# Performance work log

Measured on AMD Instinct MI355X. Metric: run time of the kernel, lower is better.

Reference implementation:

```python
import jax, jax.numpy as jnp
import numpy as np

B, IN_CS = 2, 32
H = W = D = 96

def conv1x1(w, v):
    # 1x1x1 Conv3d without bias: per-voxel matvec over channels
    return jnp.einsum('oc,bcxyz->boxyz', w, v)

def kron(a, b):
    # per-voxel outer product over channels; index order i*c2+j matches torch view
    bs, c1 = a.shape[:2]
    c2 = b.shape[1]
    out = jnp.einsum('bixyz,bjxyz->bijxyz', a, b)
    return out.reshape(bs, c1 * c2, *a.shape[2:])

def setup_inputs() -> dict:
    key = jax.random.key(0)
    ks = jax.random.split(key, 7)
    s = 0.1  # weight init scale
    return {
        'x': jax.random.normal(ks[0], (B, IN_CS, H, W, D), jnp.float32),
        'd_all': jax.random.normal(ks[1], (B, 6, H, W, D), jnp.float32),
        'W1': jax.random.normal(ks[2], (16, 2), jnp.float32) * s,
        'W2': jax.random.normal(ks[3], (3, 16), jnp.float32) * s,
        'G1': jax.random.normal(ks[4], (IN_CS, 27), jnp.float32) * s,
        'G2': jax.random.normal(ks[5], (2 * IN_CS, IN_CS), jnp.float32) * s,
        'G3': jax.random.normal(ks[6], (IN_CS, 2 * IN_CS), jnp.float32) * s,
    }

def reference(x, d_all, W1, W2, G1, G2, G3):
    def encode(v):
        return conv1x1(W2, jax.nn.relu(conv1x1(W1, v)))
    x_x = encode(d_all[:, 0:2])
    y_y = encode(d_all[:, 2:4])
    z_z = encode(d_all[:, 4:6])
    enced = kron(kron(x_x, y_y), z_z)  # [B, 27, H, W, D]
    h = jax.nn.relu(conv1x1(G1, enced))
    h = jax.nn.relu(conv1x1(G2, h))
    filters = conv1x1(G3, h)  # [B, IN_CS, H, W, D]
    return jnp.sum(x * filters, axis=1, keepdims=True)
```

## Files before the change

kernel.cpp:

```cpp
#include <hip/hip_runtime.h>


typedef _Float16 f16x8 __attribute__((ext_vector_type(8)));
typedef float    f32x4 __attribute__((ext_vector_type(4)));

constexpr int V3   = 96 * 96 * 96;
constexpr int NVOX = 2 * V3;
constexpr int TV   = 256;
constexpr int NBLK = NVOX / TV;

constexpr float SCALE     = 16384.f;
constexpr float INV_SCALE = 1.f / 16384.f;

constexpr int S32 = 40;
constexpr int S64 = 72;

__global__ __launch_bounds__(256) void metaclf_mfma(
    const float* __restrict__ x,
    const float* __restrict__ d_all,
    const float* __restrict__ W1,
    const float* __restrict__ W2,
    const float* __restrict__ G1,
    const float* __restrict__ G2,
    const float* __restrict__ G3,
    float* __restrict__ out)
{
    __shared__ _Float16 ldsA[TV * S64];
    __shared__ _Float16 ldsB[TV * S32];

    const int t    = threadIdx.x;
    const int lane = t & 63;
    const int wave = t >> 6;
    const int n16  = lane & 15;
    const int quad = lane >> 4;

    const int gidx = blockIdx.x * TV + t;
    const int b = (gidx >= V3) ? 1 : 0;
    const int v = gidx - b * V3;

    {
        float e[3][3];
#pragma unroll
        for (int a = 0; a < 3; ++a) {
            const float d0 = d_all[(b * 6 + 2 * a    ) * V3 + v];
            const float d1 = d_all[(b * 6 + 2 * a + 1) * V3 + v];
            float a0 = 0.f, a1 = 0.f, a2 = 0.f;
#pragma unroll
            for (int k = 0; k < 16; ++k) {
                const float tt = fmaxf(fmaf(W1[k * 2], d0, W1[k * 2 + 1] * d1), 0.f);
                a0 = fmaf(W2[0 * 16 + k], tt, a0);
                a1 = fmaf(W2[1 * 16 + k], tt, a1);
                a2 = fmaf(W2[2 * 16 + k], tt, a2);
            }
            e[a][0] = a0; e[a][1] = a1; e[a][2] = a2;
        }
        _Float16 row[32];
#pragma unroll
        for (int i = 0; i < 3; ++i)
#pragma unroll
            for (int j = 0; j < 3; ++j) {
                const float p = e[0][i] * e[1][j] * SCALE;
#pragma unroll
                for (int k = 0; k < 3; ++k)
                    row[i * 9 + j * 3 + k] = (_Float16)(p * e[2][k]);
            }
#pragma unroll
        for (int m = 27; m < 32; ++m) row[m] = (_Float16)0.f;

        f16x8* dst = (f16x8*)&ldsA[t * S32];
#pragma unroll
        for (int i = 0; i < 4; ++i) dst[i] = ((const f16x8*)row)[i];
    }
    __syncthreads();

    const int g0 = wave * 4;

    {
        f16x8 w0, w1;
#pragma unroll
        for (int j = 0; j < 8; ++j) {
            const int k = quad * 8 + j;
            w0[j] = (_Float16)((k < 27) ? G1[(n16     ) * 27 + k] : 0.f);
            w1[j] = (_Float16)((k < 27) ? G1[(16 + n16) * 27 + k] : 0.f);
        }
#pragma unroll
        for (int g = 0; g < 4; ++g) {
            const int rowv = (g0 + g) * 16;
            const f16x8 a = *(const f16x8*)&ldsA[(rowv + n16) * S32 + quad * 8];
            f32x4 c0 = {0.f, 0.f, 0.f, 0.f}, c1 = {0.f, 0.f, 0.f, 0.f};
            c0 = __builtin_amdgcn_mfma_f32_16x16x32_f16(a, w0, c0, 0, 0, 0);
            c1 = __builtin_amdgcn_mfma_f32_16x16x32_f16(a, w1, c1, 0, 0, 0);
#pragma unroll
            for (int r = 0; r < 4; ++r) {
                const int vr = rowv + quad * 4 + r;
                ldsB[vr * S32 + n16     ] = (_Float16)fmaxf(c0[r], 0.f);
                ldsB[vr * S32 + 16 + n16] = (_Float16)fmaxf(c1[r], 0.f);
            }
        }
    }
    __syncthreads();

    {
        f16x8 w[4];
#pragma unroll
        for (int q = 0; q < 4; ++q)
#pragma unroll
            for (int j = 0; j < 8; ++j)
                w[q][j] = (_Float16)G2[(q * 16 + n16) * 32 + quad * 8 + j];
#pragma unroll
        for (int g = 0; g < 4; ++g) {
            const int rowv = (g0 + g) * 16;
            const f16x8 a = *(const f16x8*)&ldsB[(rowv + n16) * S32 + quad * 8];
            f32x4 c[4];
#pragma unroll
            for (int q = 0; q < 4; ++q) {
                c[q] = (f32x4){0.f, 0.f, 0.f, 0.f};
                c[q] = __builtin_amdgcn_mfma_f32_16x16x32_f16(a, w[q], c[q], 0, 0, 0);
            }
#pragma unroll
            for (int r = 0; r < 4; ++r) {
                const int vr = rowv + quad * 4 + r;
#pragma unroll
                for (int q = 0; q < 4; ++q)
                    ldsA[vr * S64 + q * 16 + n16] = (_Float16)fmaxf(c[q][r], 0.f);
            }
        }
    }
    __syncthreads();

    {
        f16x8 w[2][2];
#pragma unroll
        for (int kh = 0; kh < 2; ++kh)
#pragma unroll
            for (int nh = 0; nh < 2; ++nh)
#pragma unroll
                for (int j = 0; j < 8; ++j)
                    w[kh][nh][j] = (_Float16)G3[(nh * 16 + n16) * 64 + kh * 32 + quad * 8 + j];
#pragma unroll
        for (int g = 0; g < 4; ++g) {
            const int rowv = (g0 + g) * 16;
            const f16x8 a0 = *(const f16x8*)&ldsA[(rowv + n16) * S64 + quad * 8];
            const f16x8 a1 = *(const f16x8*)&ldsA[(rowv + n16) * S64 + 32 + quad * 8];
            f32x4 c0 = {0.f, 0.f, 0.f, 0.f}, c1 = {0.f, 0.f, 0.f, 0.f};
            c0 = __builtin_amdgcn_mfma_f32_16x16x32_f16(a0, w[0][0], c0, 0, 0, 0);
            c0 = __builtin_amdgcn_mfma_f32_16x16x32_f16(a1, w[1][0], c0, 0, 0, 0);
            c1 = __builtin_amdgcn_mfma_f32_16x16x32_f16(a0, w[0][1], c1, 0, 0, 0);
            c1 = __builtin_amdgcn_mfma_f32_16x16x32_f16(a1, w[1][1], c1, 0, 0, 0);
#pragma unroll
            for (int r = 0; r < 4; ++r) {
                const int vr = rowv + quad * 4 + r;
                ldsB[vr * S32 + n16     ] = (_Float16)c0[r];
                ldsB[vr * S32 + 16 + n16] = (_Float16)c1[r];
            }
        }
    }
    __syncthreads();

    {
        f16x8 frow[4];
#pragma unroll
        for (int i = 0; i < 4; ++i)
            frow[i] = *(const f16x8*)&ldsB[t * S32 + i * 8];

        const float* xb = x + (size_t)(b * 32) * V3 + v;
        float sum = 0.f;
#pragma unroll
        for (int c = 0; c < 32; ++c) {
            const float fc = (float)frow[c / 8][c % 8];
            sum = fmaf(xb[(size_t)c * V3], fc, sum);
        }
        out[b * V3 + v] = sum * INV_SCALE;
    }
}

extern "C" void kernel_launch(void* const* d_in, const int* in_sizes, int n_in,
                              void* d_out, int out_size, void* d_ws, size_t ws_size,
                              hipStream_t stream) {
    const float* x     = (const float*)d_in[0];
    const float* d_all = (const float*)d_in[1];
    const float* W1    = (const float*)d_in[2];
    const float* W2    = (const float*)d_in[3];
    const float* G1    = (const float*)d_in[4];
    const float* G2    = (const float*)d_in[5];
    const float* G3    = (const float*)d_in[6];
    float* out = (float*)d_out;

    metaclf_mfma<<<NBLK, 256, 0, stream>>>(x, d_all, W1, W2, G1, G2, G3, out);
}
```

Before: 411.6 us.

## Share one LDS buffer, replace block barriers with wave fences, prepack weight fragments

Every wave only reads back LDS rows its own lanes wrote. The block-wide __syncthreads barriers are therefore replaced with s_waitcnt lgkmcnt(0) fences. The two LDS buffers are merged into a single buffer with a 72-element stride, which lowers shared memory per block and should let more blocks run on each CU. A small pack_weights kernel writes the G1/G2/G3 fp16 MFMA fragments to the workspace once, so each block loads them with vector loads instead of scattered fp32 loads and converts. The final filters are also kept in fp32 in LDS, and the path adds an extra kernel launch plus a dependence on lockstep execution within a wave.

```diff
diff --git a/kernel.cpp b/kernel.cpp
--- a/kernel.cpp
+++ b/kernel.cpp
@@ -8,14 +8,54 @@
 constexpr int NVOX = 2 * V3;
 constexpr int TV   = 256;
 constexpr int NBLK = NVOX / TV;
+constexpr int S    = 72;
+constexpr int SD   = 36;
 
 constexpr float SCALE     = 16384.f;
 constexpr float INV_SCALE = 1.f / 16384.f;
 
-constexpr int S32 = 40;
-constexpr int S64 = 72;
-
-__global__ __launch_bounds__(256) void metaclf_mfma(
+constexpr int N_TILES  = 10;
+constexpr int WS_BYTES = N_TILES * 64 * 8 * 2;
+
+#define LDS_FENCE() asm volatile("s_waitcnt lgkmcnt(0)" ::: "memory")
+
+__device__ __forceinline__ f16x8 build_frag(int tile, int n16, int quad,
+                                            const float* __restrict__ G1,
+                                            const float* __restrict__ G2,
+                                            const float* __restrict__ G3) {
+    f16x8 v;
+    const int k0 = quad * 8;
+#pragma unroll
+    for (int j = 0; j < 8; ++j) {
+        float f = 0.f;
+        const int k = k0 + j;
+        if (tile < 2) {
+            if (k < 27) f = G1[(tile * 16 + n16) * 27 + k];
+        } else if (tile < 6) {
+            f = G2[((tile - 2) * 16 + n16) * 32 + k];
+        } else {
+            const int kh = (tile - 6) >> 1, nh = (tile - 6) & 1;
+            f = G3[(nh * 16 + n16) * 64 + kh * 32 + k];
+        }
+        v[j] = (_Float16)f;
+    }
+    return v;
+}
+
+__global__ __launch_bounds__(256) void pack_weights(
+    const float* __restrict__ G1, const float* __restrict__ G2,
+    const float* __restrict__ G3, _Float16* __restrict__ wf)
+{
+    for (int slot = threadIdx.x; slot < N_TILES * 64; slot += 256) {
+        const int tile = slot >> 6;
+        const int lane = slot & 63;
+        const f16x8 v = build_frag(tile, lane & 15, lane >> 4, G1, G2, G3);
+        *(f16x8*)&wf[slot * 8] = v;
+    }
+}
+
+template <bool USE_WS>
+__global__ __launch_bounds__(256) void metaclf_mfma2(
     const float* __restrict__ x,
     const float* __restrict__ d_all,
     const float* __restrict__ W1,
@@ -23,20 +63,27 @@
     const float* __restrict__ G1,
     const float* __restrict__ G2,
     const float* __restrict__ G3,
+    const _Float16* __restrict__ wf,
     float* __restrict__ out)
 {
-    __shared__ _Float16 ldsA[TV * S64];
-    __shared__ _Float16 ldsB[TV * S32];
+    __shared__ _Float16 lds[TV * S];
+    float* const ldsf = (float*)lds;
 
     const int t    = threadIdx.x;
     const int lane = t & 63;
     const int wave = t >> 6;
     const int n16  = lane & 15;
     const int quad = lane >> 4;
+    const int g0   = wave * 4;
 
     const int gidx = blockIdx.x * TV + t;
     const int b = (gidx >= V3) ? 1 : 0;
     const int v = gidx - b * V3;
+
+    auto frag = [&](int tile) -> f16x8 {
+        if constexpr (USE_WS) return *(const f16x8*)&wf[(tile * 64 + lane) * 8];
+        else                  return build_frag(tile, n16, quad, G1, G2, G3);
+    };
 
     {
         float e[3][3];
@@ -67,50 +114,40 @@
 #pragma unroll
         for (int m = 27; m < 32; ++m) row[m] = (_Float16)0.f;
 
-        f16x8* dst = (f16x8*)&ldsA[t * S32];
+        f16x8* dst = (f16x8*)&lds[t * S];
 #pragma unroll
         for (int i = 0; i < 4; ++i) dst[i] = ((const f16x8*)row)[i];
     }
-    __syncthreads();
-
-    const int g0 = wave * 4;
-
-    {
-        f16x8 w0, w1;
-#pragma unroll
-        for (int j = 0; j < 8; ++j) {
-            const int k = quad * 8 + j;
-            w0[j] = (_Float16)((k < 27) ? G1[(n16     ) * 27 + k] : 0.f);
-            w1[j] = (_Float16)((k < 27) ? G1[(16 + n16) * 27 + k] : 0.f);
-        }
+    LDS_FENCE();
+
+    {
+        const f16x8 b0 = frag(0);
+        const f16x8 b1 = frag(1);
 #pragma unroll
         for (int g = 0; g < 4; ++g) {
             const int rowv = (g0 + g) * 16;
-            const f16x8 a = *(const f16x8*)&ldsA[(rowv + n16) * S32 + quad * 8];
+            const f16x8 a = *(const f16x8*)&lds[(rowv + n16) * S + quad * 8];
             f32x4 c0 = {0.f, 0.f, 0.f, 0.f}, c1 = {0.f, 0.f, 0.f, 0.f};
-            c0 = __builtin_amdgcn_mfma_f32_16x16x32_f16(a, w0, c0, 0, 0, 0);
-            c1 = __builtin_amdgcn_mfma_f32_16x16x32_f16(a, w1, c1, 0, 0, 0);
+            c0 = __builtin_amdgcn_mfma_f32_16x16x32_f16(a, b0, c0, 0, 0, 0);
+            c1 = __builtin_amdgcn_mfma_f32_16x16x32_f16(a, b1, c1, 0, 0, 0);
 #pragma unroll
             for (int r = 0; r < 4; ++r) {
                 const int vr = rowv + quad * 4 + r;
-                ldsB[vr * S32 + n16     ] = (_Float16)fmaxf(c0[r], 0.f);
-                ldsB[vr * S32 + 16 + n16] = (_Float16)fmaxf(c1[r], 0.f);
-            }
-        }
-    }
-    __syncthreads();
+                lds[vr * S + n16     ] = (_Float16)fmaxf(c0[r], 0.f);
+                lds[vr * S + 16 + n16] = (_Float16)fmaxf(c1[r], 0.f);
+            }
+        }
+    }
+    LDS_FENCE();
 
     {
         f16x8 w[4];
 #pragma unroll
-        for (int q = 0; q < 4; ++q)
-#pragma unroll
-            for (int j = 0; j < 8; ++j)
-                w[q][j] = (_Float16)G2[(q * 16 + n16) * 32 + quad * 8 + j];
+        for (int q = 0; q < 4; ++q) w[q] = frag(2 + q);
 #pragma unroll
         for (int g = 0; g < 4; ++g) {
             const int rowv = (g0 + g) * 16;
-            const f16x8 a = *(const f16x8*)&ldsB[(rowv + n16) * S32 + quad * 8];
+            const f16x8 a = *(const f16x8*)&lds[(rowv + n16) * S + quad * 8];
             f32x4 c[4];
 #pragma unroll
             for (int q = 0; q < 4; ++q) {
@@ -122,53 +159,43 @@
                 const int vr = rowv + quad * 4 + r;
 #pragma unroll
                 for (int q = 0; q < 4; ++q)
-                    ldsA[vr * S64 + q * 16 + n16] = (_Float16)fmaxf(c[q][r], 0.f);
-            }
-        }
-    }
-    __syncthreads();
-
-    {
-        f16x8 w[2][2];
-#pragma unroll
-        for (int kh = 0; kh < 2; ++kh)
-#pragma unroll
-            for (int nh = 0; nh < 2; ++nh)
-#pragma unroll
-                for (int j = 0; j < 8; ++j)
-                    w[kh][nh][j] = (_Float16)G3[(nh * 16 + n16) * 64 + kh * 32 + quad * 8 + j];
+                    lds[vr * S + q * 16 + n16] = (_Float16)fmaxf(c[q][r], 0.f);
+            }
+        }
+    }
+    LDS_FENCE();
+
+    {
+        const f16x8 w00 = frag(6), w01 = frag(7), w10 = frag(8), w11 = frag(9);
 #pragma unroll
         for (int g = 0; g < 4; ++g) {
             const int rowv = (g0 + g) * 16;
-            const f16x8 a0 = *(const f16x8*)&ldsA[(rowv + n16) * S64 + quad * 8];
-            const f16x8 a1 = *(const f16x8*)&ldsA[(rowv + n16) * S64 + 32 + quad * 8];
+            const f16x8 a0 = *(const f16x8*)&lds[(rowv + n16) * S + quad * 8];
+            const f16x8 a1 = *(const f16x8*)&lds[(rowv + n16) * S + 32 + quad * 8];
             f32x4 c0 = {0.f, 0.f, 0.f, 0.f}, c1 = {0.f, 0.f, 0.f, 0.f};
-            c0 = __builtin_amdgcn_mfma_f32_16x16x32_f16(a0, w[0][0], c0, 0, 0, 0);
-            c0 = __builtin_amdgcn_mfma_f32_16x16x32_f16(a1, w[1][0], c0, 0, 0, 0);
-            c1 = __builtin_amdgcn_mfma_f32_16x16x32_f16(a0, w[0][1], c1, 0, 0, 0);
-            c1 = __builtin_amdgcn_mfma_f32_16x16x32_f16(a1, w[1][1], c1, 0, 0, 0);
+            c0 = __builtin_amdgcn_mfma_f32_16x16x32_f16(a0, w00, c0, 0, 0, 0);
+            c0 = __builtin_amdgcn_mfma_f32_16x16x32_f16(a1, w10, c0, 0, 0, 0);
+            c1 = __builtin_amdgcn_mfma_f32_16x16x32_f16(a0, w01, c1, 0, 0, 0);
+            c1 = __builtin_amdgcn_mfma_f32_16x16x32_f16(a1, w11, c1, 0, 0, 0);
 #pragma unroll
             for (int r = 0; r < 4; ++r) {
                 const int vr = rowv + quad * 4 + r;
-                ldsB[vr * S32 + n16     ] = (_Float16)c0[r];
-                ldsB[vr * S32 + 16 + n16] = (_Float16)c1[r];
-            }
-        }
-    }
-    __syncthreads();
-
-    {
-        f16x8 frow[4];
-#pragma unroll
-        for (int i = 0; i < 4; ++i)
-            frow[i] = *(const f16x8*)&ldsB[t * S32 + i * 8];
-
+                ldsf[vr * SD + n16     ] = c0[r];
+                ldsf[vr * SD + 16 + n16] = c1[r];
+            }
+        }
+    }
+    LDS_FENCE();
+
+    {
         const float* xb = x + (size_t)(b * 32) * V3 + v;
         float sum = 0.f;
 #pragma unroll
-        for (int c = 0; c < 32; ++c) {
-            const float fc = (float)frow[c / 8][c % 8];
-            sum = fmaf(xb[(size_t)c * V3], fc, sum);
+        for (int i = 0; i < 8; ++i) {
+            const f32x4 f = *(const f32x4*)&ldsf[t * SD + i * 4];
+#pragma unroll
+            for (int r = 0; r < 4; ++r)
+                sum = fmaf(xb[(size_t)(i * 4 + r) * V3], f[r], sum);
         }
         out[b * V3 + v] = sum * INV_SCALE;
     }
@@ -186,5 +213,13 @@
     const float* G3    = (const float*)d_in[6];
     float* out = (float*)d_out;
 
-    metaclf_mfma<<<NBLK, 256, 0, stream>>>(x, d_all, W1, W2, G1, G2, G3, out);
-}
+    if (ws_size >= (size_t)WS_BYTES) {
+        _Float16* wf = (_Float16*)d_ws;
+        pack_weights<<<1, 256, 0, stream>>>(G1, G2, G3, wf);
+        metaclf_mfma2<true><<<NBLK, 256, 0, stream>>>(
+            x, d_all, W1, W2, G1, G2, G3, wf, out);
+    } else {
+        metaclf_mfma2<false><<<NBLK, 256, 0, stream>>>(
+            x, d_all, W1, W2, G1, G2, G3, nullptr, out);
+    }
+}
```

New measurement: 352.4 us. 14.4% less time.
